# Optimization experiments

Hardware: AMD Instinct MI355X
Metric: run time of the kernel (lower is better)

Reference implementation:

```python
import jax, jax.numpy as jnp
import numpy as np
import math

HEAD_SIZE = 64
BN_EPS = 1e-5  # BatchNorm eval with default running stats (mean=0, var=1)


def _rope_tables(seq_len, d):
    pos = jnp.arange(seq_len, dtype=jnp.float32)[:, None]
    div = jnp.exp(jnp.arange(0, d, 2, dtype=jnp.float32) * (-math.log(10000.0) / d))
    cos_pos = jnp.repeat(jnp.cos(pos * div), 2, axis=-1)  # [n, d]
    sin_pos = jnp.repeat(jnp.sin(pos * div), 2, axis=-1)  # [n, d]
    return cos_pos, sin_pos


def _rope(x, cos_pos, sin_pos):
    # interleaved rotation: (x0,x1) -> (-x1, x0)
    x2 = jnp.stack([-x[..., 1::2], x[..., ::2]], axis=-1).reshape(x.shape)
    return x * cos_pos + x2 * sin_pos


def _cbam(x, mlp_w1, mlp_b1, mlp_w2, mlp_b2, conv_w):
    # Channel gate: shared MLP over avg- and max-pooled [b, c] descriptors
    def mlp(v):
        return jax.nn.relu(v @ mlp_w1 + mlp_b1) @ mlp_w2 + mlp_b2
    avg = x.mean(axis=(2, 3))
    mx = x.max(axis=(2, 3))
    scale = jax.nn.sigmoid(mlp(avg) + mlp(mx))[:, :, None, None]
    x = x * scale
    # Spatial gate: 7x7 conv over channel-pooled (max, mean) maps
    comp = jnp.stack([x.max(axis=1), x.mean(axis=1)], axis=1)  # [b, 2, m, n]
    conv = jax.lax.conv_general_dilated(
        comp, conv_w, window_strides=(1, 1), padding=[(3, 3), (3, 3)],
        dimension_numbers=('NCHW', 'OIHW', 'NCHW'))
    conv = conv / jnp.sqrt(jnp.float32(1.0 + BN_EPS))  # identity BatchNorm (eval)
    return x * jax.nn.sigmoid(conv)


def setup_inputs() -> dict:
    key = jax.random.key(0)
    ks = jax.random.split(key, 12)
    b, n, h, c, d = 2, 512, 768, 108, HEAD_SIZE
    s = 0.02
    return {
        'inputs': jax.random.normal(ks[0], (b, n, h), jnp.float32),
        'event_inputs': jax.random.normal(ks[1], (c, h), jnp.float32),
        'mask': jnp.ones((b, n), jnp.int32),
        'w_dense': jax.random.normal(ks[2], (h, 2 * d), jnp.float32) * s,
        'b_dense': jax.random.normal(ks[3], (2 * d,), jnp.float32) * s,
        'w_event': jax.random.normal(ks[4], (h, d), jnp.float32) * s,
        'b_event': jax.random.normal(ks[5], (d,), jnp.float32) * s,
        'mlp_w1': jax.random.normal(ks[6], (c, c // 16), jnp.float32) * s,
        'mlp_b1': jax.random.normal(ks[7], (c // 16,), jnp.float32) * s,
        'mlp_w2': jax.random.normal(ks[8], (c // 16, c), jnp.float32) * s,
        'mlp_b2': jax.random.normal(ks[9], (c,), jnp.float32) * s,
        'conv_w': jax.random.normal(ks[10], (1, 2, 7, 7), jnp.float32) * s,
    }


def reference(inputs, event_inputs, mask, w_dense, b_dense, w_event, b_event,
              mlp_w1, mlp_b1, mlp_w2, mlp_b2, conv_w):
    b, n, _ = inputs.shape
    seq = inputs @ w_dense + b_dense          # [b, n, 2*d]
    ev = event_inputs @ w_event + b_event     # [c, d]
    qw, kw = seq[..., :HEAD_SIZE], seq[..., HEAD_SIZE:]
    cos_pos, sin_pos = _rope_tables(n, HEAD_SIZE)
    qw = _rope(qw, cos_pos, sin_pos)
    kw = _rope(kw, cos_pos, sin_pos)
    # event_output is broadcast over batch, so bcd collapses to cd
    logits = jnp.einsum('bmd,bnd,cd->bcmn', qw, kw, ev)
    logits = _cbam(logits, mlp_w1, mlp_b1, mlp_w2, mlp_b2, conv_w) + logits
    pad = (1 - mask).astype(bool)
    neg_inf = jnp.float32(-jnp.inf)
    logits = jnp.where(pad[:, None, :, None], neg_inf, logits)
    logits = jnp.where(pad[:, None, None, :], neg_inf, logits)
    tril_pen = jnp.tril(jnp.ones((n, n), logits.dtype), -1) * jnp.float32(1e12)
    logits = logits - tril_pen
    return logits / (HEAD_SIZE ** 0.5)
```

## Files before the change

### kernel.cpp

```cpp
#include <hip/hip_runtime.h>

constexpr int nB = 2;
constexpr int nS = 512;
constexpr int nH = 768;
constexpr int nC = 108;
constexpr int nD = 64;
constexpr int nBC = nB * nC;
constexpr long long nSS = (long long)nS * nS;

constexpr size_t QW_OFF    = 0;
constexpr size_t KW_OFF    = QW_OFF + (size_t)nB*nS*nD;
constexpr size_t EV_OFF    = KW_OFF + (size_t)nB*nS*nD;
constexpr size_t MAX_OFF   = EV_OFF + (size_t)nC*nD;
constexpr size_t SCALE_OFF = MAX_OFF + nBC;
constexpr size_t COMP_OFF  = SCALE_OFF + nBC;
constexpr size_t SIG_OFF   = COMP_OFF + (size_t)nB*2*nS*nS;
constexpr size_t SQK_OFF   = SIG_OFF;

typedef __attribute__((ext_vector_type(8))) short short8;
typedef __attribute__((ext_vector_type(4))) float f32x4;
union UFrag { uint4 u; short8 s; };

__device__ inline void atomicMaxF(float* addr, float v) {
    if (v >= 0.f) atomicMax((int*)addr, __float_as_int(v));
    else          atomicMin((unsigned int*)addr, __float_as_uint(v));
}

__device__ inline unsigned pack2bf(float a, float b) {
    unsigned ua = __float_as_uint(a), ub = __float_as_uint(b);
    ua = (ua + 0x7FFFu + ((ua >> 16) & 1u)) >> 16;
    ub = (ub + 0x7FFFu + ((ub >> 16) & 1u)) >> 16;
    return ua | (ub << 16);
}

__global__ __launch_bounds__(256) void k1_proj(
    const float* __restrict__ in, const float* __restrict__ evin,
    const float* __restrict__ wd, const float* __restrict__ bd,
    const float* __restrict__ we, const float* __restrict__ be,
    float* __restrict__ ws)
{
    __shared__ float rowT[nH][4];
    __shared__ float accS[2][4][128];
    __shared__ float ropeS[2][4][64];
    const int blk = blockIdx.x, tid = threadIdx.x;
    if (blk == 0 && tid < nBC) ws[MAX_OFF + tid] = -INFINITY;
    if (blk < 256) {
        const int b = blk >> 7;
        const int m0 = (blk & 127) << 2;
        const float* src = in + ((size_t)(b * nS + m0)) * nH;
        for (int q = tid; q < 4 * nH; q += 256) {
            const int r = q / nH, k = q - r * nH;
            rowT[k][r] = src[q];
        }
        __syncthreads();
        const int h = tid >> 7, c = tid & 127;
        float a0 = h ? 0.f : bd[c], a1 = 0.f, a2 = 0.f, a3 = 0.f;
        const float* wp = wd + (size_t)(h * 384) * 128 + c;
        for (int k = h * 384; k < h * 384 + 384; ++k, wp += 128) {
            const float w = *wp;
            const float4 rv = *(const float4*)&rowT[k][0];
            a0 += rv.x * w; a1 += rv.y * w; a2 += rv.z * w; a3 += rv.w * w;
        }
        accS[h][0][c] = a0; accS[h][1][c] = a1; accS[h][2][c] = a2; accS[h][3][c] = a3;
        __syncthreads();
        const int r = tid >> 6, j = tid & 63;
        const int m = m0 + r;
        const int p = j >> 1;
        const float div = expf(-0.28782313662425572f * (float)p);
        const float ang = (float)m * div;
        const float co = cosf(ang), si = sinf(ang);
#pragma unroll
        for (int half = 0; half < 2; ++half) {
            const int i0 = half * 64 + (j & ~1);
            const int i1 = half * 64 + (j | 1);
            const float x0 = accS[0][r][i0] + accS[1][r][i0];
            const float x1 = accS[0][r][i1] + accS[1][r][i1];
            const float v = (j & 1) ? (x1 * co + x0 * si) : (x0 * co - x1 * si);
            ws[(half ? KW_OFF : QW_OFF) + ((size_t)(b * nS + m)) * nD + j] = v;
            ropeS[half][r][j] = v;
        }
        __syncthreads();
        if (tid < 128) {
            const int half = tid >> 6, jj = tid & 63;
            const float t = ropeS[half][0][jj] + ropeS[half][1][jj]
                          + ropeS[half][2][jj] + ropeS[half][3][jj];
            atomicAdd(&ws[SQK_OFF + b * 128 + half * 64 + jj], t);
        }
    } else {
        const int ci = blk - 256;
        float* evrow = &rowT[0][0];
        for (int k = tid; k < nH; k += 256) evrow[k] = evin[(size_t)ci * nH + k];
        __syncthreads();
        const int c = tid & 63, h = tid >> 6;
        float acc = 0.f;
        for (int k = h * 192; k < h * 192 + 192; ++k) acc += evrow[k] * we[k * nD + c];
        accS[0][h][c] = acc;
        __syncthreads();
        if (tid < nD) {
            const float s = be[tid] + accS[0][0][tid] + accS[0][1][tid]
                          + accS[0][2][tid] + accS[0][3][tid];
            ws[EV_OFF + (size_t)ci * nD + tid] = s;
        }
    }
}

__device__ inline void stage_ev(const float* __restrict__ ws, uint4* evS, int tid) {
    for (int idx = tid; idx < 112 * 8; idx += 256) {
        const int row = idx >> 3, g = idx & 7;
        uint4 u = make_uint4(0, 0, 0, 0);
        if (row < nC) {
            const float* ep = ws + EV_OFF + row * nD + g * 8;
            float4 a = *(const float4*)ep;
            float4 b = *(const float4*)(ep + 4);
            u.x = pack2bf(a.x, a.y); u.y = pack2bf(a.z, a.w);
            u.z = pack2bf(b.x, b.y); u.w = pack2bf(b.z, b.w);
        }
        evS[row * 8 + (g ^ (row & 7))] = u;
    }
}

__device__ inline void stage_qk(const float* __restrict__ ws, float (*qkS)[68],
                                int b, int m0, int n0, int tid) {
    for (int idx = tid; idx < 64 * 16; idx += 256) {
        const int row = idx >> 4, d4 = (idx & 15) * 4;
        const float* src = (row < 32)
            ? (ws + QW_OFF + ((size_t)(b * nS + m0 + row)) * nD + d4)
            : (ws + KW_OFF + ((size_t)(b * nS + n0 + (row - 32))) * nD + d4);
        const float4 v = *(const float4*)src;
        qkS[row][d4 + 0] = v.x; qkS[row][d4 + 1] = v.y;
        qkS[row][d4 + 2] = v.z; qkS[row][d4 + 3] = v.w;
    }
}

__device__ inline void build_U(const float (*qkS)[68], uint4* U, int si, int sj, int tid) {
    const float* qr = qkS[si * 16 + (tid >> 4)];
    const float* kr = qkS[32 + sj * 16 + (tid & 15)];
#pragma unroll
    for (int g = 0; g < 8; ++g) {
        uint4 u;
        u.x = pack2bf(qr[g*8+0]*kr[g*8+0], qr[g*8+1]*kr[g*8+1]);
        u.y = pack2bf(qr[g*8+2]*kr[g*8+2], qr[g*8+3]*kr[g*8+3]);
        u.z = pack2bf(qr[g*8+4]*kr[g*8+4], qr[g*8+5]*kr[g*8+5]);
        u.w = pack2bf(qr[g*8+6]*kr[g*8+6], qr[g*8+7]*kr[g*8+7]);
        U[tid * 8 + (g ^ (tid & 7))] = u;
    }
}

__global__ __launch_bounds__(256) void kS_stats(float* __restrict__ ws)
{
    __shared__ uint4 evS[112 * 8];
    __shared__ uint4 U[256 * 8];
    __shared__ float qkS[64][68];
    __shared__ float mS[4][112];

    const int tid = threadIdx.x;
    const int b = blockIdx.y;
    const int m0 = (blockIdx.x >> 4) * 32, n0 = (blockIdx.x & 15) * 32;
    const int lane = tid & 63, w = tid >> 6;
    const int fr = lane & 15, fg = lane >> 4;

    stage_ev(ws, evS, tid);
    stage_qk(ws, qkS, b, m0, n0, tid);

    float pmax[28];
#pragma unroll
    for (int i = 0; i < 28; ++i) pmax[i] = -INFINITY;

    for (int st = 0; st < 4; ++st) {
        __syncthreads();
        build_U(qkS, U, st >> 1, st & 1, tid);
        __syncthreads();

        short8 uf[4][2];
#pragma unroll
        for (int nf = 0; nf < 4; ++nf)
#pragma unroll
            for (int ks = 0; ks < 2; ++ks) {
                const int row = w * 64 + nf * 16 + fr;
                UFrag u; u.u = U[row * 8 + ((ks * 4 + fg) ^ (row & 7))];
                uf[nf][ks] = u.s;
            }
#pragma unroll
        for (int cf = 0; cf < 7; ++cf) {
            short8 ef[2];
#pragma unroll
            for (int ks = 0; ks < 2; ++ks) {
                const int row = cf * 16 + fr;
                UFrag u; u.u = evS[row * 8 + ((ks * 4 + fg) ^ (row & 7))];
                ef[ks] = u.s;
            }
            f32x4 acc[4] = {};
#pragma unroll
            for (int ks = 0; ks < 2; ++ks)
#pragma unroll
                for (int nf = 0; nf < 4; ++nf)
                    acc[nf] = __builtin_amdgcn_mfma_f32_16x16x32_bf16(ef[ks], uf[nf][ks], acc[nf], 0, 0, 0);
#pragma unroll
            for (int nf = 0; nf < 4; ++nf)
#pragma unroll
                for (int r = 0; r < 4; ++r)
                    pmax[cf * 4 + r] = fmaxf(pmax[cf * 4 + r], acc[nf][r]);
        }
    }

#pragma unroll
    for (int i = 0; i < 28; ++i) {
#pragma unroll
        for (int off = 1; off < 16; off <<= 1)
            pmax[i] = fmaxf(pmax[i], __shfl_xor(pmax[i], off, 64));
    }
    if (fr == 0) {
#pragma unroll
        for (int cf = 0; cf < 7; ++cf)
#pragma unroll
            for (int r = 0; r < 4; ++r)
                mS[w][cf * 16 + fg * 4 + r] = pmax[cf * 4 + r];
    }
    __syncthreads();
    if (tid < nC) {
        const float mx = fmaxf(fmaxf(mS[0][tid], mS[1][tid]), fmaxf(mS[2][tid], mS[3][tid]));
        atomicMaxF(&ws[MAX_OFF + b * nC + tid], mx);
    }
}

__global__ __launch_bounds__(256) void kC_comp(
    float* __restrict__ ws, const float* __restrict__ w1, const float* __restrict__ b1,
    const float* __restrict__ w2, const float* __restrict__ b2)
{
    __shared__ uint4 evS[112 * 8];
    __shared__ uint4 U[256 * 8];
    __shared__ float qkS[64][68];
    __shared__ float hS[12], scS[112];
    __shared__ float prodS[64], avgS[112];

    const int tid = threadIdx.x;
    const int b = blockIdx.y;
    const int m0 = (blockIdx.x >> 4) * 32, n0 = (blockIdx.x & 15) * 32;

    {
        const int mlo = m0 > 3 ? m0 - 3 : 0;
        const int ncut = ((mlo >> 7) << 7) - 3;
        if (n0 + 31 < ncut) return;
    }

    const int lane = tid & 63, w = tid >> 6;
    const int fr = lane & 15, fg = lane >> 4;

    if (tid < 64) {
        const float sq = ws[SQK_OFF + b * 128 + tid];
        const float sk = ws[SQK_OFF + b * 128 + 64 + tid];
        prodS[tid] = sq * sk;
    }
    stage_ev(ws, evS, tid);
    stage_qk(ws, qkS, b, m0, n0, tid);
    __syncthreads();
    if (tid < nC) {
        const float* ep = ws + EV_OFF + (size_t)tid * nD;
        float a = 0.f;
#pragma unroll 8
        for (int d = 0; d < nD; ++d) a += ep[d] * prodS[d];
        avgS[tid] = a * (1.f / (float)nSS);
    }
    __syncthreads();
    if (tid < 12) {
        const int src = tid / 6, j = tid % 6;
        float acc = b1[j];
        if (src == 0) {
            for (int cc = 0; cc < nC; ++cc) acc += avgS[cc] * w1[cc * 6 + j];
        } else {
            const float* v = ws + MAX_OFF + b * nC;
            for (int cc = 0; cc < nC; ++cc) acc += v[cc] * w1[cc * 6 + j];
        }
        hS[tid] = fmaxf(acc, 0.f);
    }
    __syncthreads();
    if (tid < 112) {
        float s = 0.f;
        if (tid < nC) {
            float acc = 2.f * b2[tid];
#pragma unroll
            for (int j = 0; j < 6; ++j) acc += (hS[j] + hS[6 + j]) * w2[j * nC + tid];
            s = 1.f / (1.f + expf(-acc));
            if (blockIdx.x == 0) ws[SCALE_OFF + b * nC + tid] = s;
        }
        scS[tid] = s;
    }

    for (int st = 0; st < 4; ++st) {
        const int si = st >> 1, sj = st & 1;
        __syncthreads();
        build_U(qkS, U, si, sj, tid);
        __syncthreads();

        short8 uf[4][2];
#pragma unroll
        for (int nf = 0; nf < 4; ++nf)
#pragma unroll
            for (int ks = 0; ks < 2; ++ks) {
                const int row = w * 64 + nf * 16 + fr;
                UFrag u; u.u = U[row * 8 + ((ks * 4 + fg) ^ (row & 7))];
                uf[nf][ks] = u.s;
            }
        float mx[4], sm[4];
#pragma unroll
        for (int nf = 0; nf < 4; ++nf) { mx[nf] = -INFINITY; sm[nf] = 0.f; }
#pragma unroll
        for (int cf = 0; cf < 7; ++cf) {
            short8 ef[2];
#pragma unroll
            for (int ks = 0; ks < 2; ++ks) {
                const int row = cf * 16 + fr;
                UFrag u; u.u = evS[row * 8 + ((ks * 4 + fg) ^ (row & 7))];
                ef[ks] = u.s;
            }
            f32x4 acc[4] = {};
#pragma unroll
            for (int ks = 0; ks < 2; ++ks)
#pragma unroll
                for (int nf = 0; nf < 4; ++nf)
                    acc[nf] = __builtin_amdgcn_mfma_f32_16x16x32_bf16(ef[ks], uf[nf][ks], acc[nf], 0, 0, 0);
            const bool valid = (cf < 6) || (fg < 3);
#pragma unroll
            for (int nf = 0; nf < 4; ++nf)
#pragma unroll
                for (int r = 0; r < 4; ++r) {
                    const float v = scS[cf * 16 + fg * 4 + r] * acc[nf][r];
                    sm[nf] += v;
                    if (valid) mx[nf] = fmaxf(mx[nf], v);
                }
        }
#pragma unroll
        for (int nf = 0; nf < 4; ++nf) {
            mx[nf] = fmaxf(mx[nf], __shfl_xor(mx[nf], 16, 64));
            mx[nf] = fmaxf(mx[nf], __shfl_xor(mx[nf], 32, 64));
            sm[nf] += __shfl_xor(sm[nf], 16, 64);
            sm[nf] += __shfl_xor(sm[nf], 32, 64);
        }
        if (fg == 0) {
#pragma unroll
            for (int nf = 0; nf < 4; ++nf) {
                const int m = m0 + si * 16 + 4 * w + nf;
                const int n = n0 + sj * 16 + fr;
                ws[COMP_OFF + (((size_t)(b * 2 + 0)) * nS + m) * nS + n] = mx[nf];
                ws[COMP_OFF + (((size_t)(b * 2 + 1)) * nS + m) * nS + n] = sm[nf] * (1.f / (float)nC);
            }
        }
    }
}

__global__ __launch_bounds__(512) void k5_conv(float* __restrict__ ws, const float* __restrict__ cw)
{
    __shared__ float S[14][520];
    __shared__ float wS[98];
    const int n = threadIdx.x;
    const int m = blockIdx.x & 511;
    const int b = blockIdx.x >> 9;
    const int n0q = (m >> 7) << 7;
    if (n < 98) wS[n] = cw[n];
    for (int idx = n; idx < 14 * 518; idx += 512) {
        const int col = idx % 518;
        const int r = idx / 518;
        const int ch = r / 7, ky = r % 7;
        const int y = m + ky - 3;
        const int x = col - 3;
        float v = 0.f;
        if (y >= 0 && y < nS && x >= n0q - 3 && x < nS)
            v = ws[COMP_OFF + (((size_t)(b * 2 + ch)) * nS + y) * nS + x];
        S[r][col] = v;
    }
    __syncthreads();
    if (n >= n0q) {
        float acc = 0.f;
#pragma unroll
        for (int r = 0; r < 14; ++r)
#pragma unroll
            for (int kx = 0; kx < 7; ++kx)
                acc += S[r][n + kx] * wS[r * 7 + kx];
        acc *= 0.9999950000374997f;
        ws[SIG_OFF + ((size_t)b * nS + m) * nS + n] = 1.f / (1.f + expf(-acc));
    }
}

__device__ inline void stage_tiles(const float* qwp, const float* kwp, const float* evp,
                                   uint4* ldsA, uint4* ldsB, int tid)
{
#pragma unroll
    for (int i = 0; i < 4; ++i) {
        const int q = tid + i * 256;
        const int row = q >> 3, g = q & 7;
        const int sw = row * 8 + (g ^ (row & 7));
        float4 x0 = *(const float4*)(qwp + row * nD + g * 8);
        float4 x1 = *(const float4*)(qwp + row * nD + g * 8 + 4);
        float4 e0 = *(const float4*)(evp + g * 8);
        float4 e1 = *(const float4*)(evp + g * 8 + 4);
        uint4 w;
        w.x = pack2bf(x0.x * e0.x, x0.y * e0.y);
        w.y = pack2bf(x0.z * e0.z, x0.w * e0.w);
        w.z = pack2bf(x1.x * e1.x, x1.y * e1.y);
        w.w = pack2bf(x1.z * e1.z, x1.w * e1.w);
        ldsA[sw] = w;
        float4 y0 = *(const float4*)(kwp + row * nD + g * 8);
        float4 y1 = *(const float4*)(kwp + row * nD + g * 8 + 4);
        uint4 v;
        v.x = pack2bf(y0.x, y0.y);
        v.y = pack2bf(y0.z, y0.w);
        v.z = pack2bf(y1.x, y1.y);
        v.w = pack2bf(y1.z, y1.w);
        ldsB[sw] = v;
    }
}

__device__ inline void mfma_tile(const uint4* ldsA, const uint4* ldsB,
                                 int wr, int wc, int fr, int fg, f32x4 acc[4][4])
{
#pragma unroll
    for (int ks = 0; ks < 2; ++ks) {
        short8 kf[4], qf[4];
#pragma unroll
        for (int i = 0; i < 4; ++i) {
            const int row = wc * 64 + i * 16 + fr;
            const int g = ks * 4 + fg;
            UFrag u; u.u = ldsB[row * 8 + (g ^ (row & 7))];
            kf[i] = u.s;
        }
#pragma unroll
        for (int j = 0; j < 4; ++j) {
            const int row = wr * 64 + j * 16 + fr;
            const int g = ks * 4 + fg;
            UFrag u; u.u = ldsA[row * 8 + (g ^ (row & 7))];
            qf[j] = u.s;
        }
#pragma unroll
        for (int i = 0; i < 4; ++i)
#pragma unroll
            for (int j = 0; j < 4; ++j)
                acc[i][j] = __builtin_amdgcn_mfma_f32_16x16x32_bf16(kf[i], qf[j], acc[i][j], 0, 0, 0);
    }
}

__global__ __launch_bounds__(256) void k6_final(
    float* __restrict__ ws, float* __restrict__ out, const int* __restrict__ mask)
{
    __shared__ uint4 ldsA[128 * 8];
    __shared__ uint4 ldsB[128 * 8];

    const int tid = threadIdx.x;
    const int mt = blockIdx.x >> 2, nt = blockIdx.x & 3;
    const int c  = blockIdx.y;
    const int b  = blockIdx.z;
    const int m0 = mt * 128, n0 = nt * 128;
    float* outb = out + (size_t)(b * nC + c) * nSS;

    if (mt > nt) {
        const float CF = -1e12f * 0.125f;
        const int rr0 = tid >> 5;
        const int nn = n0 + (tid & 31) * 4;
        const int4 mc = *(const int4*)(mask + b * nS + nn);
#pragma unroll
        for (int p = 0; p < 16; ++p) {
            const int m = m0 + p * 8 + rr0;
            const int mr = mask[b * nS + m];
            float4 v;
            v.x = (mr && mc.x) ? CF : -INFINITY;
            v.y = (mr && mc.y) ? CF : -INFINITY;
            v.z = (mr && mc.z) ? CF : -INFINITY;
            v.w = (mr && mc.w) ? CF : -INFINITY;
            *(float4*)(outb + (size_t)m * nS + nn) = v;
        }
        return;
    }

    stage_tiles(ws + QW_OFF + ((size_t)(b * nS + m0)) * nD,
                ws + KW_OFF + ((size_t)(b * nS + n0)) * nD,
                ws + EV_OFF + (size_t)c * nD, ldsA, ldsB, tid);
    __syncthreads();

    const int lane = tid & 63;
    const int wv = tid >> 6;
    const int wr = wv >> 1, wc = wv & 1;
    const int fr = lane & 15, fg = lane >> 4;

    f32x4 acc[4][4] = {};
    mfma_tile(ldsA, ldsB, wr, wc, fr, fg, acc);

    const float scale = ws[SCALE_OFF + b * nC + c];
    const float* sig = ws + SIG_OFF + (size_t)b * nS * nS;

#pragma unroll
    for (int i = 0; i < 4; ++i) {
#pragma unroll
        for (int j = 0; j < 4; ++j) {
            const int m = m0 + wr * 64 + j * 16 + fr;
            const int nb = n0 + wc * 64 + i * 16 + fg * 4;
            const float4 sg = *(const float4*)(sig + (size_t)m * nS + nb);
            const int mrow = mask[b * nS + m];
            const int4 mcol = *(const int4*)(mask + b * nS + nb);
            const f32x4 a = acc[i][j];
            float r[4];
            const float sgv[4] = { sg.x, sg.y, sg.z, sg.w };
            const int mcv[4] = { mcol.x, mcol.y, mcol.z, mcol.w };
#pragma unroll
            for (int rr = 0; rr < 4; ++rr) {
                float v = a[rr] * (1.f + scale * sgv[rr]);
                if (!mrow || !mcv[rr]) v = -INFINITY;
                if (m > nb + rr) v -= 1e12f;
                r[rr] = v * 0.125f;
            }
            *(float4*)(outb + (size_t)m * nS + nb) = make_float4(r[0], r[1], r[2], r[3]);
        }
    }
}

extern "C" void kernel_launch(void* const* d_in, const int* in_sizes, int n_in,
                              void* d_out, int out_size, void* d_ws, size_t ws_size,
                              hipStream_t stream)
{
    const float* inputs = (const float*)d_in[0];
    const float* evin   = (const float*)d_in[1];
    const int*   mask   = (const int*)d_in[2];
    const float* wd     = (const float*)d_in[3];
    const float* bd     = (const float*)d_in[4];
    const float* we     = (const float*)d_in[5];
    const float* be     = (const float*)d_in[6];
    const float* w1     = (const float*)d_in[7];
    const float* b1     = (const float*)d_in[8];
    const float* w2     = (const float*)d_in[9];
    const float* b2     = (const float*)d_in[10];
    const float* cw     = (const float*)d_in[11];
    float* out = (float*)d_out;
    float* ws  = (float*)d_ws;

    hipMemsetAsync((char*)d_ws + SQK_OFF * sizeof(float), 0, 256 * sizeof(float), stream);
    k1_proj<<<256 + nC, 256, 0, stream>>>(inputs, evin, wd, bd, we, be, ws);
    kS_stats<<<dim3(256, nB), 256, 0, stream>>>(ws);
    kC_comp<<<dim3(256, nB), 256, 0, stream>>>(ws, w1, b1, w2, b2);
    k5_conv<<<nB * nS, 512, 0, stream>>>(ws, cw);
    k6_final<<<dim3(16, nC, nB), 256, 0, stream>>>(ws, out, mask);
}
```

Baseline: 170.1 us.

## Replace SQK atomics with partials, trim conv staging, skip masked diagonal MFMAs

```diff
diff --git a/kernel.cpp b/kernel.cpp
--- a/kernel.cpp
+++ b/kernel.cpp
@@ -84,7 +84,7 @@
             const int half = tid >> 6, jj = tid & 63;
             const float t = ropeS[half][0][jj] + ropeS[half][1][jj]
                           + ropeS[half][2][jj] + ropeS[half][3][jj];
-            atomicAdd(&ws[SQK_OFF + b * 128 + half * 64 + jj], t);
+            ws[SQK_OFF + ((size_t)(b * 128 + (blk & 127))) * 128 + half * 64 + jj] = t;
         }
     } else {
         const int ci = blk - 256;
@@ -247,8 +247,12 @@
     const int fr = lane & 15, fg = lane >> 4;
 
     if (tid < 64) {
-        const float sq = ws[SQK_OFF + b * 128 + tid];
-        const float sk = ws[SQK_OFF + b * 128 + 64 + tid];
+        const float* p = ws + SQK_OFF + (size_t)b * 128 * 128;
+        float sq = 0.f, sk = 0.f;
+        for (int blk = 0; blk < 128; ++blk) {
+            sq += p[blk * 128 + tid];
+            sk += p[blk * 128 + 64 + tid];
+        }
         prodS[tid] = sq * sk;
     }
     stage_ev(ws, evS, tid);
@@ -356,15 +360,17 @@
     const int m = blockIdx.x & 511;
     const int b = blockIdx.x >> 9;
     const int n0q = (m >> 7) << 7;
+    const int c0 = n0q;
+    const int W = 518 - c0;
     if (n < 98) wS[n] = cw[n];
-    for (int idx = n; idx < 14 * 518; idx += 512) {
-        const int col = idx % 518;
-        const int r = idx / 518;
+    for (int idx = n; idx < 14 * W; idx += 512) {
+        const int col = c0 + idx % W;
+        const int r = idx / W;
         const int ch = r / 7, ky = r % 7;
         const int y = m + ky - 3;
         const int x = col - 3;
         float v = 0.f;
-        if (y >= 0 && y < nS && x >= n0q - 3 && x < nS)
+        if (y >= 0 && y < nS && x >= 0 && x < nS)
             v = ws[COMP_OFF + (((size_t)(b * 2 + ch)) * nS + y) * nS + x];
         S[r][col] = v;
     }
@@ -411,7 +417,7 @@
 }
 
 __device__ inline void mfma_tile(const uint4* ldsA, const uint4* ldsB,
-                                 int wr, int wc, int fr, int fg, f32x4 acc[4][4])
+                                 int wr, int wc, int fr, int fg, bool diag, f32x4 acc[4][4])
 {
 #pragma unroll
     for (int ks = 0; ks < 2; ++ks) {
@@ -434,7 +440,8 @@
         for (int i = 0; i < 4; ++i)
 #pragma unroll
             for (int j = 0; j < 4; ++j)
-                acc[i][j] = __builtin_amdgcn_mfma_f32_16x16x32_bf16(kf[i], qf[j], acc[i][j], 0, 0, 0);
+                if (!diag || (wr * 64 + j * 16) <= (wc * 64 + i * 16))
+                    acc[i][j] = __builtin_amdgcn_mfma_f32_16x16x32_bf16(kf[i], qf[j], acc[i][j], 0, 0, 0);
     }
 }
 
@@ -450,9 +457,9 @@
     const int b  = blockIdx.z;
     const int m0 = mt * 128, n0 = nt * 128;
     float* outb = out + (size_t)(b * nC + c) * nSS;
+    const float CF = -1e12f * 0.125f;
 
     if (mt > nt) {
-        const float CF = -1e12f * 0.125f;
         const int rr0 = tid >> 5;
         const int nn = n0 + (tid & 31) * 4;
         const int4 mc = *(const int4*)(mask + b * nS + nn);
@@ -469,6 +476,7 @@
         }
         return;
     }
+    const bool diag = (mt == nt);
 
     stage_tiles(ws + QW_OFF + ((size_t)(b * nS + m0)) * nD,
                 ws + KW_OFF + ((size_t)(b * nS + n0)) * nD,
@@ -481,7 +489,7 @@
     const int fr = lane & 15, fg = lane >> 4;
 
     f32x4 acc[4][4] = {};
-    mfma_tile(ldsA, ldsB, wr, wc, fr, fg, acc);
+    mfma_tile(ldsA, ldsB, wr, wc, fr, fg, diag, acc);
 
     const float scale = ws[SCALE_OFF + b * nC + c];
     const float* sig = ws + SIG_OFF + (size_t)b * nS * nS;
@@ -492,19 +500,25 @@
         for (int j = 0; j < 4; ++j) {
             const int m = m0 + wr * 64 + j * 16 + fr;
             const int nb = n0 + wc * 64 + i * 16 + fg * 4;
-            const float4 sg = *(const float4*)(sig + (size_t)m * nS + nb);
             const int mrow = mask[b * nS + m];
             const int4 mcol = *(const int4*)(mask + b * nS + nb);
-            const f32x4 a = acc[i][j];
+            const int mcv[4] = { mcol.x, mcol.y, mcol.z, mcol.w };
             float r[4];
-            const float sgv[4] = { sg.x, sg.y, sg.z, sg.w };
-            const int mcv[4] = { mcol.x, mcol.y, mcol.z, mcol.w };
-#pragma unroll
-            for (int rr = 0; rr < 4; ++rr) {
-                float v = a[rr] * (1.f + scale * sgv[rr]);
-                if (!mrow || !mcv[rr]) v = -INFINITY;
-                if (m > nb + rr) v -= 1e12f;
-                r[rr] = v * 0.125f;
+            if (diag && (wr * 64 + j * 16) > (wc * 64 + i * 16)) {
+#pragma unroll
+                for (int rr = 0; rr < 4; ++rr)
+                    r[rr] = (mrow && mcv[rr]) ? CF : -INFINITY;
+            } else {
+                const float4 sg = *(const float4*)(sig + (size_t)m * nS + nb);
+                const float sgv[4] = { sg.x, sg.y, sg.z, sg.w };
+                const f32x4 a = acc[i][j];
+#pragma unroll
+                for (int rr = 0; rr < 4; ++rr) {
+                    float v = a[rr] * (1.f + scale * sgv[rr]);
+                    if (!mrow || !mcv[rr]) v = -INFINITY;
+                    if (m > nb + rr) v -= 1e12f;
+                    r[rr] = v * 0.125f;
+                }
             }
             *(float4*)(outb + (size_t)m * nS + nb) = make_float4(r[0], r[1], r[2], r[3]);
         }
@@ -530,7 +544,6 @@
     float* out = (float*)d_out;
     float* ws  = (float*)d_ws;
 
-    hipMemsetAsync((char*)d_ws + SQK_OFF * sizeof(float), 0, 256 * sizeof(float), stream);
     k1_proj<<<256 + nC, 256, 0, stream>>>(inputs, evin, wd, bd, we, be, ws);
     kS_stats<<<dim3(256, nB), 256, 0, stream>>>(ws);
     kC_comp<<<dim3(256, nB), 256, 0, stream>>>(ws, w1, b1, w2, b2);
```

New measurement: 161.0 us. 5.3% less time.
